# Kernel optimization log

Measured on AMD Instinct MI355X. Metric: run time of the kernel, lower is better.

The kernel has to match this reference:

```python
import jax, jax.numpy as jnp
import numpy as np

B, T = 4, 8
H, W = 120, 160
NON_SEM = 4
CAT = 16
MAP_CH = NON_SEM + CAT          # 20 map channels
FEAT_CH = 2 * NON_SEM + CAT     # 24 feature channels
RES = 5.0                       # cm per map cell
GLOBAL_M, LOCAL_M = 960, 240    # map_size/resolution, and /downscale
M2 = LOCAL_M * LOCAL_M
HFOV = 79.0
CAM_H_CM = 88.0
VISION_CM = 100 * RES           # vision_range cells -> cm
AGENT_R2 = 2.0 ** 2
EXPLORE_R2 = 3.0 ** 2
FX = W / (2.0 * float(np.tan(np.deg2rad(HFOV) / 2.0)))
FY = FX
CX, CY = W / 2.0, H / 2.0

LOCAL_POSE0 = jnp.array([LOCAL_M * RES / 2, LOCAL_M * RES / 2, 0.0], jnp.float32)
GLOBAL_POSE0 = jnp.array([GLOBAL_M * RES / 2, GLOBAL_M * RES / 2, 0.0], jnp.float32)
OFF = (GLOBAL_M - LOCAL_M) // 2
BOUNDS0 = jnp.array([OFF, OFF + LOCAL_M, OFF, OFF + LOCAL_M], jnp.int32)
ORIGINS0 = jnp.array([OFF * RES, OFF * RES, 0.0], jnp.float32)


def _splat1(flat, w):  # scatter-add scalar weights into the flattened local grid
    return jnp.zeros((M2,), jnp.float32).at[flat].add(w)


def _splatC(flat, vals):  # vals [C, N] -> [C, M2]
    return jnp.zeros((vals.shape[0], M2), jnp.float32).at[:, flat].add(vals)


def _step(carry, xs):
    lmap, gmap, lpose, gpose, bounds, origins = carry
    obs, delta, cam_T, done, upd = xs
    doneb = done != 0
    # per-env reset on episode end (init_map_and_pose_for_env)
    lmap = jnp.where(doneb[:, None, None, None], 0.0, lmap)
    gmap = jnp.where(doneb[:, None, None, None], 0.0, gmap)
    lpose = jnp.where(doneb[:, None], LOCAL_POSE0, lpose)
    gpose = jnp.where(doneb[:, None], GLOBAL_POSE0, gpose)
    bounds = jnp.where(doneb[:, None], BOUNDS0, bounds)
    origins = jnp.where(doneb[:, None], ORIGINS0, origins)

    # dead-reckoning pose update (delta in agent frame)
    th = jnp.deg2rad(lpose[:, 2])
    dx = delta[:, 0] * jnp.cos(th) - delta[:, 1] * jnp.sin(th)
    dy = delta[:, 0] * jnp.sin(th) + delta[:, 1] * jnp.cos(th)
    lpose = lpose + jnp.stack([dx, dy, delta[:, 2]], -1)

    # depth -> camera-frame point cloud (cm)
    depth = obs[:, 3] * 400.0 + 50.0  # [B,H,W]
    sem = obs[:, NON_SEM:]            # [B,CAT,H,W]
    uu = (jnp.arange(W, dtype=jnp.float32) - CX)[None, None, :]
    vv = (CY - jnp.arange(H, dtype=jnp.float32))[None, :, None]
    pts = jnp.stack([uu * depth / FX, vv * depth / FY, depth, jnp.ones_like(depth)], -1)
    pts = jnp.einsum('bij,bhwj->bhwi', cam_T, pts)  # camera extrinsics
    x_f, y_l, z_u = pts[..., 2], -pts[..., 0], pts[..., 1] + CAM_H_CM

    # agent frame -> local map frame
    th2 = jnp.deg2rad(lpose[:, 2])[:, None, None]
    wx = lpose[:, 0][:, None, None] + x_f * jnp.cos(th2) - y_l * jnp.sin(th2)
    wy = lpose[:, 1][:, None, None] + x_f * jnp.sin(th2) + y_l * jnp.cos(th2)
    ix = jnp.floor(wx / RES).astype(jnp.int32)
    iy = jnp.floor(wy / RES).astype(jnp.int32)
    valid = (depth > 25.0) & (depth < VISION_CM) & (ix >= 0) & (ix < LOCAL_M) & (iy >= 0) & (iy < LOCAL_M)
    flat = (jnp.clip(iy, 0, LOCAL_M - 1) * LOCAL_M + jnp.clip(ix, 0, LOCAL_M - 1)).reshape(B, -1)
    vm = valid.reshape(B, -1).astype(jnp.float32)
    obst_w = vm * ((z_u > 25.0) & (z_u < 150.0)).reshape(B, -1).astype(jnp.float32)

    exp_grid = jax.vmap(_splat1)(flat, vm).reshape(B, LOCAL_M, LOCAL_M)
    obst_grid = jax.vmap(_splat1)(flat, obst_w).reshape(B, LOCAL_M, LOCAL_M)
    sem_grid = jax.vmap(_splatC)(flat, sem.reshape(B, CAT, -1) * vm[:, None, :]).reshape(B, CAT, LOCAL_M, LOCAL_M)

    # agent location / been-close disks
    g = jnp.arange(LOCAL_M, dtype=jnp.float32)
    dxg = g[None, None, :] - (lpose[:, 0] / RES)[:, None, None]
    dyg = g[None, :, None] - (lpose[:, 1] / RES)[:, None, None]
    d2 = dxg * dxg + dyg * dyg
    agent = (d2 <= AGENT_R2).astype(jnp.float32)
    close = (d2 <= EXPLORE_R2).astype(jnp.float32)

    lmap = jnp.concatenate([
        jnp.maximum(lmap[:, 0], jnp.clip(obst_grid, 0.0, 1.0))[:, None],
        jnp.maximum(lmap[:, 1], jnp.clip(exp_grid, 0.0, 1.0))[:, None],
        agent[:, None],
        jnp.maximum(lmap[:, 3], close)[:, None],
        jnp.maximum(lmap[:, NON_SEM:], jnp.clip(sem_grid, 0.0, 1.0)),
    ], axis=1)

    # fuse local window into global map for envs flagged for update
    y1, x1 = bounds[:, 0], bounds[:, 2]
    crop = jax.vmap(lambda gm, y, x: jax.lax.dynamic_slice(gm, (0, y, x), (MAP_CH, LOCAL_M, LOCAL_M)))(gmap, y1, x1)
    updb = (upd != 0)[:, None, None, None]
    fused = jnp.where(updb, jnp.maximum(crop, lmap), crop)
    gmap = jax.vmap(lambda gm, c, y, x: jax.lax.dynamic_update_slice(gm, c, (0, y, x)))(gmap, fused, y1, x1)
    gpose = jnp.where((upd != 0)[:, None], lpose + origins, gpose)

    feats = jnp.concatenate([lmap[:, :NON_SEM], fused[:, :NON_SEM], lmap[:, NON_SEM:]], axis=1)
    return (lmap, gmap, lpose, gpose, bounds, origins), (feats, lpose, gpose, bounds, origins)


def _forward(obs_seq, pose_delta, cam_poses, init_local_map, init_global_map,
             init_local_pose, init_global_pose, init_origins,
             done_flags, update_flags, init_bounds):
    xs = (obs_seq.swapaxes(0, 1), pose_delta.swapaxes(0, 1), cam_poses.swapaxes(0, 1),
          done_flags.swapaxes(0, 1), update_flags.swapaxes(0, 1))
    carry0 = (init_local_map, init_global_map, init_local_pose, init_global_pose, init_bounds, init_origins)
    carry, ys = jax.lax.scan(_step, carry0, xs)
    feats, lp, gp, bnds, orgs = ys
    return (feats.swapaxes(0, 1), carry[0], carry[1], lp.swapaxes(0, 1), gp.swapaxes(0, 1),
            bnds.swapaxes(0, 1), orgs.swapaxes(0, 1))


def setup_inputs() -> dict:
    key = jax.random.key(0)
    ks = jax.random.split(key, 5)
    obs_seq = jax.random.uniform(ks[0], (B, T, MAP_CH, H, W), jnp.float32)
    pose_delta = jax.random.normal(ks[1], (B, T, 3), jnp.float32) * jnp.array([10.0, 2.0, 5.0], jnp.float32)
    cam_poses = jnp.eye(4, dtype=jnp.float32)[None, None] + 0.02 * jax.random.normal(ks[2], (B, T, 4, 4), jnp.float32)
    done_flags = jax.random.randint(ks[3], (B, T), 0, 2, jnp.int32)
    update_flags = jax.random.randint(ks[4], (B, T), 0, 2, jnp.int32)
    return {
        'obs_seq': obs_seq,
        'pose_delta': pose_delta,
        'done_flags': done_flags,
        'update_flags': update_flags,
        'cam_poses': cam_poses,
        'init_local_map': jnp.zeros((B, MAP_CH, LOCAL_M, LOCAL_M), jnp.float32),
        'init_global_map': jnp.zeros((B, MAP_CH, GLOBAL_M, GLOBAL_M), jnp.float32),
        'init_local_pose': jnp.tile(LOCAL_POSE0[None], (B, 1)),
        'init_global_pose': jnp.tile(GLOBAL_POSE0[None], (B, 1)),
        'init_bounds': jnp.tile(BOUNDS0[None], (B, 1)),
        'init_origins': jnp.tile(ORIGINS0[None], (B, 1)),
    }


def reference(obs_seq, pose_delta, done_flags, update_flags, cam_poses,
              init_local_map, init_global_map, init_local_pose, init_global_pose,
              init_bounds, init_origins):
    return _forward(obs_seq, pose_delta, cam_poses, init_local_map, init_global_map,
                    init_local_pose, init_global_pose, init_origins,
                    done_flags, update_flags, init_bounds)
```

## Files before the change

### kernel.cpp

```cpp
#include <hip/hip_runtime.h>
#include <math.h>

#define Bn 4
#define Tn 8
#define Hn 120
#define Wn 160
#define HWn (Hn * Wn)
#define NON_SEMn 4
#define CATn 16
#define MAP_CHn 20
#define FEAT_CHn 24
#define LOCAL_Mn 240
#define GLOBAL_Mn 960
#define M2n (LOCAL_Mn * LOCAL_Mn)
#define TBMn (Tn * Bn * M2n)
#define Pn (Tn * Bn * HWn)
#define NBLK_SCAN 1800
#define UPD_BLKS ((Bn * M2n + 255) / 256)
#define GMAP_BLKS ((Bn * MAP_CHn * GLOBAL_Mn * GLOBAL_Mn / 4 + 255) / 256)

#define DEG2RADf ((float)0.017453292519943295)

typedef float vf4 __attribute__((ext_vector_type(4)));

#define OUT_FEATS 0
#define OUT_LMAP  44236800
#define OUT_GMAP  48844800
#define OUT_LP    122572800
#define OUT_GP    122572896
#define OUT_BNDS  122572992
#define OUT_ORGS  122573120

#define WS_LPOSE  0
#define WS_ANYD   96
#define WS_REC4   128
#define WS_BSUM   (WS_REC4 + 4 * TBMn)
#define WS_CELL   (WS_BSUM + 2048)
#define WS_LIST   (WS_CELL + Pn)
#define WS_RECS   (WS_LIST + Pn)


__global__ void pose_kernel(const float* __restrict__ pose_delta,
                            const int* __restrict__ done_flags,
                            const int* __restrict__ upd_flags,
                            const float* __restrict__ init_lpose,
                            const float* __restrict__ init_gpose,
                            const int* __restrict__ init_bounds,
                            const float* __restrict__ init_origins,
                            float* __restrict__ ws_lpose,
                            float* __restrict__ ws_anydone,
                            float* __restrict__ out_lp,
                            float* __restrict__ out_gp,
                            float* __restrict__ out_bnds,
                            float* __restrict__ out_orgs) {
#pragma clang fp contract(off)
    int b = threadIdx.x;
    if (b >= Bn) return;
    float lx = init_lpose[b * 3 + 0], ly = init_lpose[b * 3 + 1], lz = init_lpose[b * 3 + 2];
    float gx = init_gpose[b * 3 + 0], gy = init_gpose[b * 3 + 1], gz = init_gpose[b * 3 + 2];
    int b0 = init_bounds[b * 4 + 0], b1 = init_bounds[b * 4 + 1];
    int b2i = init_bounds[b * 4 + 2], b3 = init_bounds[b * 4 + 3];
    float ox = init_origins[b * 3 + 0], oy = init_origins[b * 3 + 1], oz = init_origins[b * 3 + 2];
    float anyd = 0.0f;
    for (int t = 0; t < Tn; t++) {
        int done = done_flags[b * Tn + t];
        int upd  = upd_flags[b * Tn + t];
        if (done) {
            lx = 600.0f; ly = 600.0f; lz = 0.0f;
            gx = 2400.0f; gy = 2400.0f; gz = 0.0f;
            b0 = 360; b1 = 600; b2i = 360; b3 = 600;
            ox = 1800.0f; oy = 1800.0f; oz = 0.0f;
            anyd = 1.0f;
        }
        float th = lz * DEG2RADf;
        float c = cosf(th), s = sinf(th);
        float d0 = pose_delta[(b * Tn + t) * 3 + 0];
        float d1 = pose_delta[(b * Tn + t) * 3 + 1];
        float d2 = pose_delta[(b * Tn + t) * 3 + 2];
        lx = lx + (d0 * c - d1 * s);
        ly = ly + (d0 * s + d1 * c);
        lz = lz + d2;
        if (upd) { gx = lx + ox; gy = ly + oy; gz = lz + oz; }
        ws_lpose[(t * Bn + b) * 3 + 0] = lx;
        ws_lpose[(t * Bn + b) * 3 + 1] = ly;
        ws_lpose[(t * Bn + b) * 3 + 2] = lz;
        out_lp[(b * Tn + t) * 3 + 0] = lx;
        out_lp[(b * Tn + t) * 3 + 1] = ly;
        out_lp[(b * Tn + t) * 3 + 2] = lz;
        out_gp[(b * Tn + t) * 3 + 0] = gx;
        out_gp[(b * Tn + t) * 3 + 1] = gy;
        out_gp[(b * Tn + t) * 3 + 2] = gz;
        out_bnds[(b * Tn + t) * 4 + 0] = (float)b0;
        out_bnds[(b * Tn + t) * 4 + 1] = (float)b1;
        out_bnds[(b * Tn + t) * 4 + 2] = (float)b2i;
        out_bnds[(b * Tn + t) * 4 + 3] = (float)b3;
        out_orgs[(b * Tn + t) * 3 + 0] = ox;
        out_orgs[(b * Tn + t) * 3 + 1] = oy;
        out_orgs[(b * Tn + t) * 3 + 2] = oz;
    }
    ws_anydone[b] = anyd;
}

__global__ void project_bin_kernel(const float* __restrict__ obs,
                                   const float* __restrict__ cam,
                                   const float* __restrict__ ws_lpose,
                                   uint4* __restrict__ rec4,
                                   int* __restrict__ cellid,
                                   float* __restrict__ recs,
                                   float fx) {
#pragma clang fp contract(off)
    int g = blockIdx.x * blockDim.x + threadIdx.x;
    if (g >= Pn) return;
    int p = g % HWn;
    int tb = g / HWn;
    int b = tb % Bn;
    int t = tb / Bn;
    int h = p / Wn, w = p % Wn;
    const float* ob = obs + (size_t)((b * Tn + t) * MAP_CHn) * HWn;
    float depth = ob[3 * HWn + p] * 400.0f + 50.0f;
    float u = (float)w - 80.0f;
    float v = 60.0f - (float)h;
    float px = u * depth / fx;
    float py = v * depth / fx;
    float pz = depth;
    const float* Tm = cam + (size_t)(b * Tn + t) * 16;
    float X = ((Tm[0] * px + Tm[1] * py) + Tm[2] * pz) + Tm[3];
    float Y = ((Tm[4] * px + Tm[5] * py) + Tm[6] * pz) + Tm[7];
    float Z = ((Tm[8] * px + Tm[9] * py) + Tm[10] * pz) + Tm[11];
    float x_f = Z;
    float y_l = -X;
    float z_u = Y + 88.0f;
    float lx = ws_lpose[(t * Bn + b) * 3 + 0];
    float ly = ws_lpose[(t * Bn + b) * 3 + 1];
    float lz = ws_lpose[(t * Bn + b) * 3 + 2];
    float th2 = lz * DEG2RADf;
    float c2 = cosf(th2), s2 = sinf(th2);
    float wx = (lx + x_f * c2) - y_l * s2;
    float wy = (ly + x_f * s2) + y_l * c2;
    int ix = (int)floorf(wx / 5.0f);
    int iy = (int)floorf(wy / 5.0f);
    bool valid = (depth > 25.0f) && (depth < 500.0f) &&
                 (ix >= 0) && (ix < LOCAL_Mn) && (iy >= 0) && (iy < LOCAL_Mn);

    vf4 r[4];
#pragma unroll
    for (int q = 0; q < 4; q++) {
        r[q].x = ob[(size_t)(NON_SEMn + 4 * q + 0) * HWn + p];
        r[q].y = ob[(size_t)(NON_SEMn + 4 * q + 1) * HWn + p];
        r[q].z = ob[(size_t)(NON_SEMn + 4 * q + 2) * HWn + p];
        r[q].w = ob[(size_t)(NON_SEMn + 4 * q + 3) * HWn + p];
    }
    vf4* rp = (vf4*)(recs + (size_t)g * CATn);
#pragma unroll
    for (int q = 0; q < 4; q++)
        __builtin_nontemporal_store(r[q], rp + q);

    int cell = -1;
    if (valid) {
        cell = (t * Bn + b) * M2n + iy * LOCAL_Mn + ix;
        float* rf = (float*)&rec4[cell];
        rf[0] = 1.0f;
        if (z_u > 25.0f && z_u < 150.0f) rf[1] = 1.0f;
        atomicAdd(((unsigned*)&rec4[cell]) + 2, 1u);
    }
    cellid[g] = cell;
}

__global__ void scan1_kernel(uint4* __restrict__ rec4,
                             unsigned* __restrict__ bsum) {
    __shared__ unsigned s[256];
    int tid = threadIdx.x;
    int base = blockIdx.x * 1024 + tid * 4;
    uint4 r0 = rec4[base], r1 = rec4[base + 1], r2 = rec4[base + 2], r3 = rec4[base + 3];
    unsigned v0 = r0.z, v1 = r1.z, v2 = r2.z, v3 = r3.z;
    unsigned tsum = v0 + v1 + v2 + v3;
    s[tid] = tsum;
    __syncthreads();
    for (int d = 1; d < 256; d <<= 1) {
        unsigned a = (tid >= d) ? s[tid - d] : 0u;
        __syncthreads();
        s[tid] += a;
        __syncthreads();
    }
    unsigned excl = s[tid] - tsum;
    if (tid == 255) bsum[blockIdx.x] = s[255];
    ((unsigned*)&rec4[base])[3]     = excl;
    ((unsigned*)&rec4[base + 1])[3] = excl + v0;
    ((unsigned*)&rec4[base + 2])[3] = excl + v0 + v1;
    ((unsigned*)&rec4[base + 3])[3] = excl + v0 + v1 + v2;
}

__global__ void scan_carry_kernel(uint4* __restrict__ rec4,
                                  const unsigned* __restrict__ bsum) {
    __shared__ unsigned ls[256];
    int tid = threadIdx.x;
    unsigned part = 0;
    for (int i = tid; i < (int)blockIdx.x; i += 256) part += bsum[i];
    ls[tid] = part;
    __syncthreads();
    for (int d = 128; d > 0; d >>= 1) {
        if (tid < d) ls[tid] += ls[tid + d];
        __syncthreads();
    }
    unsigned carry = ls[0];
    if (carry == 0) return;
    int base = blockIdx.x * 1024 + tid * 4;
#pragma unroll
    for (int k = 0; k < 4; k++) {
        unsigned* wp = ((unsigned*)&rec4[base + k]) + 3;
        *wp = *wp + carry;
    }
}

__global__ void scatter_kernel(const int* __restrict__ cellid,
                               uint4* __restrict__ rec4,
                               unsigned* __restrict__ list) {
    int g = blockIdx.x * blockDim.x + threadIdx.x;
    if (g >= Pn) return;
    int c = cellid[g];
    if (c < 0) return;
    unsigned pos = atomicAdd(((unsigned*)&rec4[c]) + 3, 1u);
    list[pos] = (unsigned)g;
}

__global__ void __launch_bounds__(256)
mega_kernel(const uint4* __restrict__ rec4,
            const unsigned* __restrict__ list,
            const float* __restrict__ recs,
            const int* __restrict__ done_flags,
            const int* __restrict__ upd_flags,
            const float* __restrict__ ws_lpose,
            const float* __restrict__ init_lmap,
            const float* __restrict__ init_gmap,
            const int* __restrict__ init_bounds,
            const float* __restrict__ anydone,
            float* __restrict__ out_feats,
            float* __restrict__ out_lmap,
            float* __restrict__ out_gmap) {
#pragma clang fp contract(off)
    if (blockIdx.x >= UPD_BLKS) {
        size_t i4 = (size_t)(blockIdx.x - UPD_BLKS) * blockDim.x + threadIdx.x;
        const size_t total4 = (size_t)Bn * MAP_CHn * GLOBAL_Mn * GLOBAL_Mn / 4;
        if (i4 >= total4) return;
        size_t f = i4 * 4;
        int gx = (int)(f % GLOBAL_Mn);
        size_t r = f / GLOBAL_Mn;
        int gy = (int)(r % GLOBAL_Mn);
        size_t bc = r / GLOBAL_Mn;
        int b = (int)(bc / MAP_CHn);
        int y1 = init_bounds[b * 4 + 0];
        int x1 = init_bounds[b * 4 + 2];
        if (gy >= y1 && gy < y1 + LOCAL_Mn && gx >= x1 && gx < x1 + LOCAL_Mn) return;
        vf4 v;
        if (anydone[b] != 0.0f) {
            v = (vf4)(0.0f);
        } else {
            v = __builtin_nontemporal_load((const vf4*)(init_gmap + f));
        }
        __builtin_nontemporal_store(v, (vf4*)(out_gmap + f));
        return;
    }

    int idx = blockIdx.x * blockDim.x + threadIdx.x;
    if (idx >= Bn * M2n) return;
    int b = idx / M2n, j = idx % M2n;
    int y = j / LOCAL_Mn, x = j % LOCAL_Mn;
    int y1 = init_bounds[b * 4 + 0];
    int x1 = init_bounds[b * 4 + 2];

    float lm[MAP_CHn], cr[MAP_CHn];
#pragma unroll
    for (int ch = 0; ch < MAP_CHn; ch++)
        lm[ch] = __builtin_nontemporal_load(init_lmap + ((size_t)(b * MAP_CHn + ch)) * M2n + j);
#pragma unroll
    for (int ch = 0; ch < MAP_CHn; ch++)
        cr[ch] = __builtin_nontemporal_load(
            init_gmap + ((size_t)(b * MAP_CHn + ch) * GLOBAL_Mn + (y1 + y)) * GLOBAL_Mn + (x1 + x));

    for (int t = 0; t < Tn; t++) {
        int done = done_flags[b * Tn + t];
        int upd  = upd_flags[b * Tn + t];
        if (done) {
#pragma unroll
            for (int ch = 0; ch < MAP_CHn; ch++) { lm[ch] = 0.0f; cr[ch] = 0.0f; }
        }
        float lx = ws_lpose[(t * Bn + b) * 3 + 0];
        float ly = ws_lpose[(t * Bn + b) * 3 + 1];
        float dxg = (float)x - lx / 5.0f;
        float dyg = (float)y - ly / 5.0f;
        float d2 = dxg * dxg + dyg * dyg;
        float agent = (d2 <= 4.0f) ? 1.0f : 0.0f;
        float close = (d2 <= 9.0f) ? 1.0f : 0.0f;

        int cell = (t * Bn + b) * M2n + j;
        uint4 rc = rec4[cell];
        float expv  = __uint_as_float(rc.x);
        float obstv = __uint_as_float(rc.y);
        unsigned n  = rc.z;
        unsigned st = rc.w - n;
        lm[0] = fmaxf(lm[0], fminf(fmaxf(obstv, 0.0f), 1.0f));
        lm[1] = fmaxf(lm[1], fminf(fmaxf(expv, 0.0f), 1.0f));
        lm[2] = agent;
        lm[3] = fmaxf(lm[3], close);

        float sem[CATn];
#pragma unroll
        for (int c = 0; c < CATn; c++) sem[c] = 0.0f;
        for (unsigned k = 0; k < n; k++) {
            unsigned g = list[st + k];
            const vf4* rp = (const vf4*)(recs + (size_t)g * CATn);
            vf4 r0 = rp[0], r1 = rp[1], r2 = rp[2], r3 = rp[3];
            sem[0] += r0.x;  sem[1] += r0.y;  sem[2] += r0.z;  sem[3] += r0.w;
            sem[4] += r1.x;  sem[5] += r1.y;  sem[6] += r1.z;  sem[7] += r1.w;
            sem[8] += r2.x;  sem[9] += r2.y;  sem[10] += r2.z; sem[11] += r2.w;
            sem[12] += r3.x; sem[13] += r3.y; sem[14] += r3.z; sem[15] += r3.w;
        }
#pragma unroll
        for (int c = 0; c < CATn; c++)
            lm[NON_SEMn + c] = fmaxf(lm[NON_SEMn + c], fminf(fmaxf(sem[c], 0.0f), 1.0f));
        if (upd) {
#pragma unroll
            for (int ch = 0; ch < MAP_CHn; ch++) cr[ch] = fmaxf(cr[ch], lm[ch]);
        }

        size_t fb = ((size_t)(b * Tn + t) * FEAT_CHn) * M2n + j;
#pragma unroll
        for (int ch = 0; ch < NON_SEMn; ch++)
            __builtin_nontemporal_store(lm[ch], out_feats + fb + (size_t)ch * M2n);
#pragma unroll
        for (int ch = 0; ch < NON_SEMn; ch++)
            __builtin_nontemporal_store(cr[ch], out_feats + fb + (size_t)(NON_SEMn + ch) * M2n);
#pragma unroll
        for (int c = 0; c < CATn; c++)
            __builtin_nontemporal_store(lm[NON_SEMn + c], out_feats + fb + (size_t)(2 * NON_SEMn + c) * M2n);
    }

#pragma unroll
    for (int ch = 0; ch < MAP_CHn; ch++)
        __builtin_nontemporal_store(lm[ch], out_lmap + ((size_t)(b * MAP_CHn + ch)) * M2n + j);
#pragma unroll
    for (int ch = 0; ch < MAP_CHn; ch++)
        __builtin_nontemporal_store(
            cr[ch], out_gmap + ((size_t)(b * MAP_CHn + ch) * GLOBAL_Mn + (y1 + y)) * GLOBAL_Mn + (x1 + x));
}

extern "C" void kernel_launch(void* const* d_in, const int* in_sizes, int n_in,
                              void* d_out, int out_size, void* d_ws, size_t ws_size,
                              hipStream_t stream) {
    const float* obs        = (const float*)d_in[0];
    const float* pose_delta = (const float*)d_in[1];
    const int*   done_flags = (const int*)d_in[2];
    const int*   upd_flags  = (const int*)d_in[3];
    const float* cam_poses  = (const float*)d_in[4];
    const float* init_lmap  = (const float*)d_in[5];
    const float* init_gmap  = (const float*)d_in[6];
    const float* init_lpose = (const float*)d_in[7];
    const float* init_gpose = (const float*)d_in[8];
    const int*   init_bnds  = (const int*)d_in[9];
    const float* init_orgs  = (const float*)d_in[10];

    float* out = (float*)d_out;
    float* ws  = (float*)d_ws;

    float*    ws_lpose = ws + WS_LPOSE;
    float*    ws_anyd  = ws + WS_ANYD;
    uint4*    rec4     = (uint4*)(ws + WS_REC4);
    unsigned* bsum     = (unsigned*)(ws + WS_BSUM);
    int*      cellid   = (int*)(ws + WS_CELL);
    unsigned* list     = (unsigned*)(ws + WS_LIST);
    float*    recs     = ws + WS_RECS;

    float fx = (float)(160.0 / (2.0 * tan(79.0 * M_PI / 180.0 / 2.0)));

    pose_kernel<<<1, 64, 0, stream>>>(pose_delta, done_flags, upd_flags,
                                      init_lpose, init_gpose, init_bnds, init_orgs,
                                      ws_lpose, ws_anyd,
                                      out + OUT_LP, out + OUT_GP,
                                      out + OUT_BNDS, out + OUT_ORGS);

    (void)hipMemsetAsync(rec4, 0, (size_t)TBMn * sizeof(uint4), stream);

    project_bin_kernel<<<(Pn + 255) / 256, 256, 0, stream>>>(
        obs, cam_poses, ws_lpose, rec4, cellid, recs, fx);

    scan1_kernel<<<NBLK_SCAN, 256, 0, stream>>>(rec4, bsum);
    scan_carry_kernel<<<NBLK_SCAN, 256, 0, stream>>>(rec4, bsum);

    scatter_kernel<<<(Pn + 255) / 256, 256, 0, stream>>>(cellid, rec4, list);

    mega_kernel<<<UPD_BLKS + GMAP_BLKS, 256, 0, stream>>>(
        rec4, list, recs, done_flags, upd_flags, ws_lpose,
        init_lmap, init_gmap, init_bnds, ws_anyd,
        out + OUT_FEATS, out + OUT_LMAP, out + OUT_GMAP);
}
```

Baseline: 920.9 us.

## Compact cell records, sort semantic rows by cell, replace carry pass with block-sum scan

Cell records shrink from uint4 to uint2: count and obstacle flag are packed into one atomic word, and the scan offset sits in the second word. The separate carry kernel is replaced by a single-block scan of the block sums, which later kernels add when they look up an offset. Semantic rows are now written directly into cell-sorted order during scatter, so the mega kernel reads them contiguously with no index list, and it skips empty cells. This cuts memset and scan traffic and removes the indirect gather. The cost is 16-bit count packing, which assumes fewer than 65536 points per cell, and a serial single-block scan.

```diff
diff --git a/kernel.cpp b/kernel.cpp
--- a/kernel.cpp
+++ b/kernel.cpp
@@ -33,11 +33,10 @@
 
 #define WS_LPOSE  0
 #define WS_ANYD   96
-#define WS_REC4   128
-#define WS_BSUM   (WS_REC4 + 4 * TBMn)
+#define WS_REC2   128
+#define WS_BSUM   (WS_REC2 + 2 * TBMn)
 #define WS_CELL   (WS_BSUM + 2048)
-#define WS_LIST   (WS_CELL + Pn)
-#define WS_RECS   (WS_LIST + Pn)
+#define WS_RECB   (WS_CELL + Pn)
 
 
 __global__ void pose_kernel(const float* __restrict__ pose_delta,
@@ -101,13 +100,12 @@
     ws_anydone[b] = anyd;
 }
 
-__global__ void project_bin_kernel(const float* __restrict__ obs,
-                                   const float* __restrict__ cam,
-                                   const float* __restrict__ ws_lpose,
-                                   uint4* __restrict__ rec4,
-                                   int* __restrict__ cellid,
-                                   float* __restrict__ recs,
-                                   float fx) {
+__global__ void project_kernel(const float* __restrict__ obs,
+                               const float* __restrict__ cam,
+                               const float* __restrict__ ws_lpose,
+                               uint2* __restrict__ rec2,
+                               int* __restrict__ cellid,
+                               float fx) {
 #pragma clang fp contract(off)
     int g = blockIdx.x * blockDim.x + threadIdx.x;
     if (g >= Pn) return;
@@ -141,38 +139,22 @@
     int iy = (int)floorf(wy / 5.0f);
     bool valid = (depth > 25.0f) && (depth < 500.0f) &&
                  (ix >= 0) && (ix < LOCAL_Mn) && (iy >= 0) && (iy < LOCAL_Mn);
-
-    vf4 r[4];
-#pragma unroll
-    for (int q = 0; q < 4; q++) {
-        r[q].x = ob[(size_t)(NON_SEMn + 4 * q + 0) * HWn + p];
-        r[q].y = ob[(size_t)(NON_SEMn + 4 * q + 1) * HWn + p];
-        r[q].z = ob[(size_t)(NON_SEMn + 4 * q + 2) * HWn + p];
-        r[q].w = ob[(size_t)(NON_SEMn + 4 * q + 3) * HWn + p];
-    }
-    vf4* rp = (vf4*)(recs + (size_t)g * CATn);
-#pragma unroll
-    for (int q = 0; q < 4; q++)
-        __builtin_nontemporal_store(r[q], rp + q);
-
     int cell = -1;
     if (valid) {
         cell = (t * Bn + b) * M2n + iy * LOCAL_Mn + ix;
-        float* rf = (float*)&rec4[cell];
-        rf[0] = 1.0f;
-        if (z_u > 25.0f && z_u < 150.0f) rf[1] = 1.0f;
-        atomicAdd(((unsigned*)&rec4[cell]) + 2, 1u);
+        unsigned addv = 1u + ((z_u > 25.0f && z_u < 150.0f) ? 65536u : 0u);
+        atomicAdd(&rec2[cell].x, addv);
     }
     cellid[g] = cell;
 }
 
-__global__ void scan1_kernel(uint4* __restrict__ rec4,
+__global__ void scan1_kernel(uint2* __restrict__ rec2,
                              unsigned* __restrict__ bsum) {
     __shared__ unsigned s[256];
     int tid = threadIdx.x;
     int base = blockIdx.x * 1024 + tid * 4;
-    uint4 r0 = rec4[base], r1 = rec4[base + 1], r2 = rec4[base + 2], r3 = rec4[base + 3];
-    unsigned v0 = r0.z, v1 = r1.z, v2 = r2.z, v3 = r3.z;
+    unsigned v0 = rec2[base].x & 0xFFFFu, v1 = rec2[base + 1].x & 0xFFFFu;
+    unsigned v2 = rec2[base + 2].x & 0xFFFFu, v3 = rec2[base + 3].x & 0xFFFFu;
     unsigned tsum = v0 + v1 + v2 + v3;
     s[tid] = tsum;
     __syncthreads();
@@ -184,49 +166,67 @@
     }
     unsigned excl = s[tid] - tsum;
     if (tid == 255) bsum[blockIdx.x] = s[255];
-    ((unsigned*)&rec4[base])[3]     = excl;
-    ((unsigned*)&rec4[base + 1])[3] = excl + v0;
-    ((unsigned*)&rec4[base + 2])[3] = excl + v0 + v1;
-    ((unsigned*)&rec4[base + 3])[3] = excl + v0 + v1 + v2;
-}
-
-__global__ void scan_carry_kernel(uint4* __restrict__ rec4,
-                                  const unsigned* __restrict__ bsum) {
-    __shared__ unsigned ls[256];
+    rec2[base].y     = excl;
+    rec2[base + 1].y = excl + v0;
+    rec2[base + 2].y = excl + v0 + v1;
+    rec2[base + 3].y = excl + v0 + v1 + v2;
+}
+
+__global__ void scan2_kernel(unsigned* __restrict__ bsum) {
+    __shared__ unsigned s[256];
     int tid = threadIdx.x;
-    unsigned part = 0;
-    for (int i = tid; i < (int)blockIdx.x; i += 256) part += bsum[i];
-    ls[tid] = part;
-    __syncthreads();
-    for (int d = 128; d > 0; d >>= 1) {
-        if (tid < d) ls[tid] += ls[tid + d];
+    unsigned run = 0;
+    for (int base = 0; base < NBLK_SCAN; base += 256) {
+        int i = base + tid;
+        unsigned v = (i < NBLK_SCAN) ? bsum[i] : 0u;
+        s[tid] = v;
         __syncthreads();
-    }
-    unsigned carry = ls[0];
-    if (carry == 0) return;
-    int base = blockIdx.x * 1024 + tid * 4;
-#pragma unroll
-    for (int k = 0; k < 4; k++) {
-        unsigned* wp = ((unsigned*)&rec4[base + k]) + 3;
-        *wp = *wp + carry;
-    }
-}
-
-__global__ void scatter_kernel(const int* __restrict__ cellid,
-                               uint4* __restrict__ rec4,
-                               unsigned* __restrict__ list) {
+        for (int d = 1; d < 256; d <<= 1) {
+            unsigned a = (tid >= d) ? s[tid - d] : 0u;
+            __syncthreads();
+            s[tid] += a;
+            __syncthreads();
+        }
+        unsigned tot = s[255];
+        if (i < NBLK_SCAN) bsum[i] = run + s[tid] - v;
+        run += tot;
+        __syncthreads();
+    }
+}
+
+__global__ void scatter_copy_kernel(const float* __restrict__ obs,
+                                    const int* __restrict__ cellid,
+                                    const unsigned* __restrict__ bsum,
+                                    uint2* __restrict__ rec2,
+                                    float* __restrict__ recb) {
     int g = blockIdx.x * blockDim.x + threadIdx.x;
     if (g >= Pn) return;
     int c = cellid[g];
     if (c < 0) return;
-    unsigned pos = atomicAdd(((unsigned*)&rec4[c]) + 3, 1u);
-    list[pos] = (unsigned)g;
+    int p = g % HWn;
+    int tb = g / HWn;
+    int b = tb % Bn;
+    int t = tb / Bn;
+    const float* ob = obs + (size_t)((b * Tn + t) * MAP_CHn) * HWn;
+    vf4 r[4];
+#pragma unroll
+    for (int q = 0; q < 4; q++) {
+        r[q].x = ob[(size_t)(NON_SEMn + 4 * q + 0) * HWn + p];
+        r[q].y = ob[(size_t)(NON_SEMn + 4 * q + 1) * HWn + p];
+        r[q].z = ob[(size_t)(NON_SEMn + 4 * q + 2) * HWn + p];
+        r[q].w = ob[(size_t)(NON_SEMn + 4 * q + 3) * HWn + p];
+    }
+    unsigned pos = bsum[c >> 10] + atomicAdd(&rec2[c].y, 1u);
+    vf4* rp = (vf4*)(recb + (size_t)pos * CATn);
+#pragma unroll
+    for (int q = 0; q < 4; q++)
+        __builtin_nontemporal_store(r[q], rp + q);
 }
 
 __global__ void __launch_bounds__(256)
-mega_kernel(const uint4* __restrict__ rec4,
-            const unsigned* __restrict__ list,
-            const float* __restrict__ recs,
+mega_kernel(const uint2* __restrict__ rec2,
+            const unsigned* __restrict__ bsum,
+            const float* __restrict__ recb,
             const int* __restrict__ done_flags,
             const int* __restrict__ upd_flags,
             const float* __restrict__ ws_lpose,
@@ -293,31 +293,31 @@
         float close = (d2 <= 9.0f) ? 1.0f : 0.0f;
 
         int cell = (t * Bn + b) * M2n + j;
-        uint4 rc = rec4[cell];
-        float expv  = __uint_as_float(rc.x);
-        float obstv = __uint_as_float(rc.y);
-        unsigned n  = rc.z;
-        unsigned st = rc.w - n;
-        lm[0] = fmaxf(lm[0], fminf(fmaxf(obstv, 0.0f), 1.0f));
-        lm[1] = fmaxf(lm[1], fminf(fmaxf(expv, 0.0f), 1.0f));
+        uint2 rc = rec2[cell];
+        unsigned n = rc.x & 0xFFFFu;
+        lm[0] = fmaxf(lm[0], (rc.x >> 16) ? 1.0f : 0.0f);
+        lm[1] = fmaxf(lm[1], n ? 1.0f : 0.0f);
         lm[2] = agent;
         lm[3] = fmaxf(lm[3], close);
 
-        float sem[CATn];
-#pragma unroll
-        for (int c = 0; c < CATn; c++) sem[c] = 0.0f;
-        for (unsigned k = 0; k < n; k++) {
-            unsigned g = list[st + k];
-            const vf4* rp = (const vf4*)(recs + (size_t)g * CATn);
-            vf4 r0 = rp[0], r1 = rp[1], r2 = rp[2], r3 = rp[3];
-            sem[0] += r0.x;  sem[1] += r0.y;  sem[2] += r0.z;  sem[3] += r0.w;
-            sem[4] += r1.x;  sem[5] += r1.y;  sem[6] += r1.z;  sem[7] += r1.w;
-            sem[8] += r2.x;  sem[9] += r2.y;  sem[10] += r2.z; sem[11] += r2.w;
-            sem[12] += r3.x; sem[13] += r3.y; sem[14] += r3.z; sem[15] += r3.w;
-        }
-#pragma unroll
-        for (int c = 0; c < CATn; c++)
-            lm[NON_SEMn + c] = fmaxf(lm[NON_SEMn + c], fminf(fmaxf(sem[c], 0.0f), 1.0f));
+        if (n) {
+            unsigned st = bsum[cell >> 10] + rc.y - n;
+            float sem[CATn];
+#pragma unroll
+            for (int c = 0; c < CATn; c++) sem[c] = 0.0f;
+            const vf4* rp = (const vf4*)(recb + (size_t)st * CATn);
+            for (unsigned k = 0; k < n; k++) {
+                vf4 r0 = rp[0], r1 = rp[1], r2 = rp[2], r3 = rp[3];
+                rp += 4;
+                sem[0] += r0.x;  sem[1] += r0.y;  sem[2] += r0.z;  sem[3] += r0.w;
+                sem[4] += r1.x;  sem[5] += r1.y;  sem[6] += r1.z;  sem[7] += r1.w;
+                sem[8] += r2.x;  sem[9] += r2.y;  sem[10] += r2.z; sem[11] += r2.w;
+                sem[12] += r3.x; sem[13] += r3.y; sem[14] += r3.z; sem[15] += r3.w;
+            }
+#pragma unroll
+            for (int c = 0; c < CATn; c++)
+                lm[NON_SEMn + c] = fmaxf(lm[NON_SEMn + c], fminf(fmaxf(sem[c], 0.0f), 1.0f));
+        }
         if (upd) {
 #pragma unroll
             for (int ch = 0; ch < MAP_CHn; ch++) cr[ch] = fmaxf(cr[ch], lm[ch]);
@@ -364,11 +364,10 @@
 
     float*    ws_lpose = ws + WS_LPOSE;
     float*    ws_anyd  = ws + WS_ANYD;
-    uint4*    rec4     = (uint4*)(ws + WS_REC4);
+    uint2*    rec2     = (uint2*)(ws + WS_REC2);
     unsigned* bsum     = (unsigned*)(ws + WS_BSUM);
     int*      cellid   = (int*)(ws + WS_CELL);
-    unsigned* list     = (unsigned*)(ws + WS_LIST);
-    float*    recs     = ws + WS_RECS;
+    float*    recb     = ws + WS_RECB;
 
     float fx = (float)(160.0 / (2.0 * tan(79.0 * M_PI / 180.0 / 2.0)));
 
@@ -378,18 +377,19 @@
                                       out + OUT_LP, out + OUT_GP,
                                       out + OUT_BNDS, out + OUT_ORGS);
 
-    (void)hipMemsetAsync(rec4, 0, (size_t)TBMn * sizeof(uint4), stream);
-
-    project_bin_kernel<<<(Pn + 255) / 256, 256, 0, stream>>>(
-        obs, cam_poses, ws_lpose, rec4, cellid, recs, fx);
-
-    scan1_kernel<<<NBLK_SCAN, 256, 0, stream>>>(rec4, bsum);
-    scan_carry_kernel<<<NBLK_SCAN, 256, 0, stream>>>(rec4, bsum);
-
-    scatter_kernel<<<(Pn + 255) / 256, 256, 0, stream>>>(cellid, rec4, list);
+    (void)hipMemsetAsync(rec2, 0, (size_t)TBMn * sizeof(uint2), stream);
+
+    project_kernel<<<(Pn + 255) / 256, 256, 0, stream>>>(
+        obs, cam_poses, ws_lpose, rec2, cellid, fx);
+
+    scan1_kernel<<<NBLK_SCAN, 256, 0, stream>>>(rec2, bsum);
+    scan2_kernel<<<1, 256, 0, stream>>>(bsum);
+
+    scatter_copy_kernel<<<(Pn + 255) / 256, 256, 0, stream>>>(
+        obs, cellid, bsum, rec2, recb);
 
     mega_kernel<<<UPD_BLKS + GMAP_BLKS, 256, 0, stream>>>(
-        rec4, list, recs, done_flags, upd_flags, ws_lpose,
+        rec2, bsum, recb, done_flags, upd_flags, ws_lpose,
         init_lmap, init_gmap, init_bnds, ws_anyd,
         out + OUT_FEATS, out + OUT_LMAP, out + OUT_GMAP);
 }
```

Result: faster. 837.4 us (-9.1%).
